# Kernel optimization log

Measured on AMD Instinct MI355X. Metric: run time of the kernel, lower is better.

## Reference

```python
import jax, jax.numpy as jnp
import numpy as np
from jax import lax

KERNEL_SIZE = 3
DIM = 64
FILTERS = 32
BATCH = 128
WIDTH = 8192
STRIDE = 1


def setup_inputs() -> dict:
    key = jax.random.key(0)
    k1, k2 = jax.random.split(key)
    x = jax.random.normal(k1, (BATCH, WIDTH, DIM), dtype=jnp.float32)
    # glorot-uniform init for the polar kernel, shape (kernel_size, dim, filters)
    fan_in = KERNEL_SIZE * DIM
    fan_out = KERNEL_SIZE * FILTERS
    limit = float(np.sqrt(6.0 / (fan_in + fan_out)))
    polar_kernel = jax.random.uniform(
        k2, (KERNEL_SIZE, DIM, FILTERS), dtype=jnp.float32,
        minval=-limit, maxval=limit)
    return {"x": x, "polar_kernel": polar_kernel}


def reference(x, polar_kernel):
    # Strided VALID 1D conv: (B, W, D) x (K, D, F) -> (B, W_out, F)
    out = lax.conv_general_dilated(
        x, polar_kernel,
        window_strides=(STRIDE,),
        padding="VALID",
        dimension_numbers=("NWC", "WIO", "NWC"))
    # expand to (B, W_out, F, 1); activation is identity (activation=None)
    out = out[..., None]
    # per-sample global min-max normalization over axes (1, 2, 3)
    mn = jnp.min(out, axis=(1, 2, 3), keepdims=True)
    mx = jnp.max(out, axis=(1, 2, 3), keepdims=True)
    return (out - mn) / (mx - mn)
```

## Files before the change

### kernel.cpp

```cpp
#include <hip/hip_runtime.h>
#include <hip/hip_bf16.h>

#define BATCH  128
#define WIDTH  8192
#define DIM    64
#define FILT   32
#define KSZ    3
#define WOUT   8190
#define RPW    30
#define WT     120
#define TPB    18
#define NBX    4

typedef __attribute__((ext_vector_type(8))) _Float16 f16x8;
typedef __attribute__((ext_vector_type(4))) float f32x4;

template<int PASS>
__global__ __launch_bounds__(256, 2)
void conv_pass(const float* __restrict__ x, const float* __restrict__ ker,
               float* __restrict__ out, float* __restrict__ mm)
{
  __shared__ __align__(16) float xs[2][4][32][DIM];
  __shared__ __align__(16) short ks[KSZ * FILT * DIM];
  __shared__ float red[8];

  const int t  = threadIdx.x;
  const int l  = t & 63;
  const int wv = t >> 6;
  const int b  = blockIdx.y;
  const int tile0 = blockIdx.x * TPB;
  const float* xb = x + (long)b * WIDTH * DIM;

  auto stage = [&](int bb, int tile) {
    long gw0 = (long)(tile0 + tile) * WT + wv * RPW;
    char* lb = (char*)&xs[bb][wv][0][0];
    #pragma unroll
    for (int j = 0; j < 8; ++j) {
      int row_l = j * 4 + (l >> 4);
      int slot  = (l & 15) ^ (row_l & 7);
      long gr = gw0 + row_l;
      if (gr > WIDTH - 1) gr = WIDTH - 1;
      __builtin_amdgcn_global_load_lds(
          (const __attribute__((address_space(1))) void*)(xb + gr * DIM + slot * 4),
          (__attribute__((address_space(3))) void*)(lb + j * 1024), 16, 0, 0);
    }
  };

  stage(0, 0);

  #pragma unroll
  for (int i = 0; i < 24; ++i) {
    int idx = t + i * 256;
    int k = idx >> 11, rem = idx & 2047;
    int d = rem >> 5,  f = rem & 31;
    _Float16 hv = (_Float16)ker[idx];
    int byte = ((k * FILT + f) * DIM + d) * 2;
    byte ^= (f & 7) << 4;
    ks[byte >> 1] = __builtin_bit_cast(short, hv);
  }
  __syncthreads();

  f16x8 Bf[KSZ][2][2];
  #pragma unroll
  for (int s = 0; s < KSZ; ++s)
    #pragma unroll
    for (int kh = 0; kh < 2; ++kh)
      #pragma unroll
      for (int nt = 0; nt < 2; ++nt) {
        int f  = nt * 16 + (l & 15);
        int d0 = kh * 32 + (l >> 4) * 8;
        int byte = ((s * FILT + f) * DIM + d0) * 2;
        byte ^= (f & 7) << 4;
        Bf[s][kh][nt] = *reinterpret_cast<const f16x8*>(&ks[byte >> 1]);
      }

  float mx = -INFINITY, mn = INFINITY;
  float mnv = 0.f, rs = 0.f;
  if (PASS == 1) {
    float mxv = -INFINITY; mnv = INFINITY;
    #pragma unroll
    for (int i = 0; i < NBX; ++i) {
      mxv = fmaxf(mxv, mm[(b * NBX + i) * 2]);
      mnv = fminf(mnv, mm[(b * NBX + i) * 2 + 1]);
    }
    rs = 1.0f / (mxv - mnv);
  }

  int cur = 0;
  for (int it = 0; it < TPB; ++it) {
    if (it + 1 < TPB) {
      stage(cur ^ 1, it + 1);
      asm volatile("s_waitcnt vmcnt(8)" ::: "memory");
    } else {
      asm volatile("s_waitcnt vmcnt(0)" ::: "memory");
    }
    __builtin_amdgcn_sched_barrier(0);

    const float* xl = &xs[cur][wv][0][0];
    f32x4 acc[2][2];
    #pragma unroll
    for (int mt = 0; mt < 2; ++mt)
      #pragma unroll
      for (int nt = 0; nt < 2; ++nt)
        acc[mt][nt] = (f32x4){0.f, 0.f, 0.f, 0.f};

    #pragma unroll
    for (int s = 0; s < KSZ; ++s) {
      #pragma unroll
      for (int kh = 0; kh < 2; ++kh) {
        f16x8 a[2];
        #pragma unroll
        for (int mt = 0; mt < 2; ++mt) {
          int r  = mt * 16 + (l & 15) + s;
          int sg = kh * 8 + (l >> 4) * 2;
          int rb = r & 7;
          f32x4 u0 = *reinterpret_cast<const f32x4*>(&xl[r * DIM + ((sg    ) ^ rb) * 4]);
          f32x4 u1 = *reinterpret_cast<const f32x4*>(&xl[r * DIM + ((sg + 1) ^ rb) * 4]);
          f16x8 av;
          av[0] = (_Float16)u0.x; av[1] = (_Float16)u0.y;
          av[2] = (_Float16)u0.z; av[3] = (_Float16)u0.w;
          av[4] = (_Float16)u1.x; av[5] = (_Float16)u1.y;
          av[6] = (_Float16)u1.z; av[7] = (_Float16)u1.w;
          a[mt] = av;
        }
        #pragma unroll
        for (int mt = 0; mt < 2; ++mt)
          #pragma unroll
          for (int nt = 0; nt < 2; ++nt)
            acc[mt][nt] = __builtin_amdgcn_mfma_f32_16x16x32_f16(
                a[mt], Bf[s][kh][nt], acc[mt][nt], 0, 0, 0);
      }
    }

    long w0t = (long)(tile0 + it) * WT + wv * RPW;
    if (PASS == 0) {
      #pragma unroll
      for (int mt = 0; mt < 2; ++mt)
        #pragma unroll
        for (int nt = 0; nt < 2; ++nt)
          #pragma unroll
          for (int r = 0; r < 4; ++r) {
            int wl = mt * 16 + (l >> 4) * 4 + r;
            long gr = w0t + wl;
            if (wl < RPW && gr < WOUT) {
              float v = acc[mt][nt][r];
              mx = fmaxf(mx, v); mn = fminf(mn, v);
            }
          }
    } else {
      #pragma unroll
      for (int mt = 0; mt < 2; ++mt)
        #pragma unroll
        for (int nt = 0; nt < 2; ++nt)
          #pragma unroll
          for (int r = 0; r < 4; ++r) {
            int wl = mt * 16 + (l >> 4) * 4 + r;
            long gr = w0t + wl;
            if (wl < RPW && gr < WOUT) {
              int f = nt * 16 + (l & 15);
              out[((long)b * WOUT + gr) * FILT + f] = (acc[mt][nt][r] - mnv) * rs;
            }
          }
    }
    cur ^= 1;
  }

  if (PASS == 0) {
    #pragma unroll
    for (int off = 32; off > 0; off >>= 1) {
      mx = fmaxf(mx, __shfl_down(mx, off));
      mn = fminf(mn, __shfl_down(mn, off));
    }
    if (l == 0) { red[wv * 2] = mx; red[wv * 2 + 1] = mn; }
    __syncthreads();
    if (t == 0) {
      float Mx = fmaxf(fmaxf(red[0], red[2]), fmaxf(red[4], red[6]));
      float Mn = fminf(fminf(red[1], red[3]), fminf(red[5], red[7]));
      mm[(b * NBX + blockIdx.x) * 2]     = Mx;
      mm[(b * NBX + blockIdx.x) * 2 + 1] = Mn;
    }
  }
}

extern "C" void kernel_launch(void* const* d_in, const int* in_sizes, int n_in,
                              void* d_out, int out_size, void* d_ws, size_t ws_size,
                              hipStream_t stream) {
  const float* x   = (const float*)d_in[0];
  const float* ker = (const float*)d_in[1];
  float* out = (float*)d_out;
  float* mm  = (float*)d_ws;

  dim3 grid(NBX, BATCH);
  conv_pass<0><<<grid, dim3(256), 0, stream>>>(x, ker, nullptr, mm);
  conv_pass<1><<<grid, dim3(256), 0, stream>>>(x, ker, out, mm);
}
```

Baseline: 137.0 us.

## Compute conv once, store raw output, normalize in separate elementwise kernel

The conv+MFMA pass used to run twice, once for per-sample min/max and once for the normalized write. Now it runs once: it writes the raw conv result into a workspace buffer while reducing min/max, and a light vectorized kernel then reads that buffer and applies the min-max scaling. This removes the second read of x and the second round of MFMA work. In exchange it adds a write and a read of the intermediate buffer, so total memory traffic stays about the same, and it assumes the workspace can hold the full conv output.

```diff
diff --git a/kernel.cpp b/kernel.cpp
--- a/kernel.cpp
+++ b/kernel.cpp
@@ -15,10 +15,9 @@
 typedef __attribute__((ext_vector_type(8))) _Float16 f16x8;
 typedef __attribute__((ext_vector_type(4))) float f32x4;
 
-template<int PASS>
 __global__ __launch_bounds__(256, 2)
-void conv_pass(const float* __restrict__ x, const float* __restrict__ ker,
-               float* __restrict__ out, float* __restrict__ mm)
+void conv_min(const float* __restrict__ x, const float* __restrict__ ker,
+              float* __restrict__ cf, float* __restrict__ mm)
 {
   __shared__ __align__(16) float xs[2][4][32][DIM];
   __shared__ __align__(16) short ks[KSZ * FILT * DIM];
@@ -75,16 +74,6 @@
       }
 
   float mx = -INFINITY, mn = INFINITY;
-  float mnv = 0.f, rs = 0.f;
-  if (PASS == 1) {
-    float mxv = -INFINITY; mnv = INFINITY;
-    #pragma unroll
-    for (int i = 0; i < NBX; ++i) {
-      mxv = fmaxf(mxv, mm[(b * NBX + i) * 2]);
-      mnv = fminf(mnv, mm[(b * NBX + i) * 2 + 1]);
-    }
-    rs = 1.0f / (mxv - mnv);
-  }
 
   int cur = 0;
   for (int it = 0; it < TPB; ++it) {
@@ -133,52 +122,62 @@
     }
 
     long w0t = (long)(tile0 + it) * WT + wv * RPW;
-    if (PASS == 0) {
+    #pragma unroll
+    for (int mt = 0; mt < 2; ++mt)
       #pragma unroll
-      for (int mt = 0; mt < 2; ++mt)
+      for (int nt = 0; nt < 2; ++nt)
         #pragma unroll
-        for (int nt = 0; nt < 2; ++nt)
-          #pragma unroll
-          for (int r = 0; r < 4; ++r) {
-            int wl = mt * 16 + (l >> 4) * 4 + r;
-            long gr = w0t + wl;
-            if (wl < RPW && gr < WOUT) {
-              float v = acc[mt][nt][r];
-              mx = fmaxf(mx, v); mn = fminf(mn, v);
-            }
+        for (int r = 0; r < 4; ++r) {
+          int wl = mt * 16 + (l >> 4) * 4 + r;
+          long gr = w0t + wl;
+          if (wl < RPW && gr < WOUT) {
+            float v = acc[mt][nt][r];
+            mx = fmaxf(mx, v); mn = fminf(mn, v);
+            int f = nt * 16 + (l & 15);
+            cf[((long)b * WOUT + gr) * FILT + f] = v;
           }
-    } else {
-      #pragma unroll
-      for (int mt = 0; mt < 2; ++mt)
-        #pragma unroll
-        for (int nt = 0; nt < 2; ++nt)
-          #pragma unroll
-          for (int r = 0; r < 4; ++r) {
-            int wl = mt * 16 + (l >> 4) * 4 + r;
-            long gr = w0t + wl;
-            if (wl < RPW && gr < WOUT) {
-              int f = nt * 16 + (l & 15);
-              out[((long)b * WOUT + gr) * FILT + f] = (acc[mt][nt][r] - mnv) * rs;
-            }
-          }
-    }
+        }
     cur ^= 1;
   }
 
-  if (PASS == 0) {
-    #pragma unroll
-    for (int off = 32; off > 0; off >>= 1) {
-      mx = fmaxf(mx, __shfl_down(mx, off));
-      mn = fminf(mn, __shfl_down(mn, off));
-    }
-    if (l == 0) { red[wv * 2] = mx; red[wv * 2 + 1] = mn; }
-    __syncthreads();
-    if (t == 0) {
-      float Mx = fmaxf(fmaxf(red[0], red[2]), fmaxf(red[4], red[6]));
-      float Mn = fminf(fminf(red[1], red[3]), fminf(red[5], red[7]));
-      mm[(b * NBX + blockIdx.x) * 2]     = Mx;
-      mm[(b * NBX + blockIdx.x) * 2 + 1] = Mn;
-    }
+  #pragma unroll
+  for (int off = 32; off > 0; off >>= 1) {
+    mx = fmaxf(mx, __shfl_down(mx, off));
+    mn = fminf(mn, __shfl_down(mn, off));
+  }
+  if (l == 0) { red[wv * 2] = mx; red[wv * 2 + 1] = mn; }
+  __syncthreads();
+  if (t == 0) {
+    float Mx = fmaxf(fmaxf(red[0], red[2]), fmaxf(red[4], red[6]));
+    float Mn = fminf(fminf(red[1], red[3]), fminf(red[5], red[7]));
+    mm[(b * NBX + blockIdx.x) * 2]     = Mx;
+    mm[(b * NBX + blockIdx.x) * 2 + 1] = Mn;
+  }
+}
+
+__global__ __launch_bounds__(256)
+void norm_out(const float* __restrict__ cf, const float* __restrict__ mm,
+              float* __restrict__ out)
+{
+  const int b = blockIdx.y;
+  float mx = -INFINITY, mn = INFINITY;
+  #pragma unroll
+  for (int i = 0; i < NBX; ++i) {
+    mx = fmaxf(mx, mm[(b * NBX + i) * 2]);
+    mn = fminf(mn, mm[(b * NBX + i) * 2 + 1]);
+  }
+  const float rs = 1.0f / (mx - mn);
+
+  const int c = blockIdx.x * 256 + threadIdx.x;
+  if (c < WOUT * 8) {
+    long base = (long)b * (WOUT * FILT) + (long)c * 4;
+    f32x4 v = *reinterpret_cast<const f32x4*>(cf + base);
+    f32x4 o;
+    o.x = (v.x - mn) * rs;
+    o.y = (v.y - mn) * rs;
+    o.z = (v.z - mn) * rs;
+    o.w = (v.w - mn) * rs;
+    *reinterpret_cast<f32x4*>(out + base) = o;
   }
 }
 
@@ -189,8 +188,8 @@
   const float* ker = (const float*)d_in[1];
   float* out = (float*)d_out;
   float* mm  = (float*)d_ws;
+  float* cf  = (float*)((char*)d_ws + 4096);
 
-  dim3 grid(NBX, BATCH);
-  conv_pass<0><<<grid, dim3(256), 0, stream>>>(x, ker, nullptr, mm);
-  conv_pass<1><<<grid, dim3(256), 0, stream>>>(x, ker, out, mm);
+  conv_min<<<dim3(NBX, BATCH), dim3(256), 0, stream>>>(x, ker, cf, mm);
+  norm_out<<<dim3(256, BATCH), dim3(256), 0, stream>>>(cf, mm, out);
 }
```

Result: faster. 133.1 us (-2.8%).
